# Performance work log

Measured on AMD Instinct MI355X. Metric: run time of the kernel, lower is better.

The kernel has to match this reference:

```python
import jax, jax.numpy as jnp
import numpy as np

N, E, G = 30000, 240000, 1500
EMB, NODE_DIM, EDGE_DIM, TASKS = 300, 9, 3, 12
L_ENC, L_RAT = 5, 2
GAMMA, T_CON = 0.4, 0.2


def _w(key, shape, fan_in):
    return jax.random.normal(key, shape, jnp.float32) / np.float32(np.sqrt(fan_in))


def setup_inputs() -> dict:
    key = jax.random.key(0)
    ks = jax.random.split(key, 32)
    inp = {}
    inp['x'] = jax.random.normal(ks[0], (N, NODE_DIM), jnp.float32)
    inp['edge_attr'] = jax.random.normal(ks[1], (E, EDGE_DIM), jnp.float32)
    inp['edge_index'] = jax.random.randint(ks[2], (2, E), 0, N, jnp.int32)
    b = jnp.sort(jax.random.randint(ks[3], (N,), 0, G, jnp.int32))
    inp['batch'] = b.at[0].set(0).at[-1].set(G - 1)
    u = jax.random.uniform(ks[4], (N, 2), jnp.float32, 1e-6, 1.0 - 1e-6)
    inp['gumbel'] = -jnp.log(-jnp.log(u))  # standard Gumbel noise (tau=1)
    inp['perm'] = jax.random.permutation(ks[5], G).astype(jnp.int32)
    inp['W_enc'] = _w(ks[6], (NODE_DIM, EMB), NODE_DIM)
    inp['b_enc'] = jnp.zeros((EMB,), jnp.float32)
    inp['We_g'] = _w(ks[7], (L_ENC, EDGE_DIM, EMB), EDGE_DIM)
    inp['be_g'] = jnp.zeros((L_ENC, EMB), jnp.float32)
    inp['W1_g'] = _w(ks[8], (L_ENC, EMB, 2 * EMB), EMB)
    inp['b1_g'] = jnp.zeros((L_ENC, 2 * EMB), jnp.float32)
    inp['W2_g'] = _w(ks[9], (L_ENC, 2 * EMB, EMB), 2 * EMB)
    inp['b2_g'] = jnp.zeros((L_ENC, EMB), jnp.float32)
    inp['We_r'] = _w(ks[10], (L_RAT, EDGE_DIM, EMB), EDGE_DIM)
    inp['be_r'] = jnp.zeros((L_RAT, EMB), jnp.float32)
    inp['W1_r'] = _w(ks[11], (L_RAT, EMB, 2 * EMB), EMB)
    inp['b1_r'] = jnp.zeros((L_RAT, 2 * EMB), jnp.float32)
    inp['W2_r'] = _w(ks[12], (L_RAT, 2 * EMB, EMB), 2 * EMB)
    inp['b2_r'] = jnp.zeros((L_RAT, EMB), jnp.float32)
    inp['Wg1'] = _w(ks[13], (EMB, 2 * EMB), EMB)
    inp['bg1'] = jnp.zeros((2 * EMB,), jnp.float32)
    inp['Wg2'] = _w(ks[14], (2 * EMB, 2), 2 * EMB)
    inp['bg2'] = jnp.zeros((2,), jnp.float32)
    inp['Wp1'] = _w(ks[15], (EMB, 2 * EMB), EMB)
    inp['bp1'] = jnp.zeros((2 * EMB,), jnp.float32)
    inp['Wp2'] = _w(ks[16], (2 * EMB, TASKS), 2 * EMB)
    inp['bp2'] = jnp.zeros((TASKS,), jnp.float32)
    return inp


def _gin_stack(x, src, dst, edge_attr, We, be, W1, b1, W2, b2):
    # GIN-style message passing with edge features, residual, JK='last'.
    L = We.shape[0]
    for l in range(L):
        e = edge_attr @ We[l] + be[l]                               # [E, EMB]
        msg = jax.nn.relu(x[src] + e)                                # gather [E, EMB]
        agg = jax.ops.segment_sum(msg, dst, num_segments=x.shape[0])  # scatter [N, EMB]
        h = jax.nn.relu((agg + x) @ W1[l] + b1[l]) @ W2[l] + b2[l]
        if l < L - 1:
            h = jax.nn.relu(h)
        x = x + h  # residual
    return x


def _mlp2(h, Wa, ba, Wb, bb):
    # Linear -> (BN=identity in eval) -> ReLU -> (Dropout=identity) -> Linear
    return jax.nn.relu(h @ Wa + ba) @ Wb + bb


def _forward(x, edge_attr, gumbel, W_enc, b_enc, We_g, be_g, W1_g, b1_g, W2_g, b2_g,
             We_r, be_r, W1_r, b1_r, W2_r, b2_r, Wg1, bg1, Wg2, bg2, Wp1, bp1, Wp2, bp2,
             edge_index, batch, perm):
    src, dst = edge_index[0], edge_index[1]
    cnt = jnp.clip(jax.ops.segment_sum(jnp.ones((x.shape[0],), jnp.float32), batch, num_segments=G), 1.0)[:, None]

    def gmean(v):
        return jax.ops.segment_sum(v, batch, num_segments=G) / cnt

    x_feat = x @ W_enc + b_enc                                      # node encoder
    h_node = _gin_stack(x_feat, src, dst, edge_attr, We_g, be_g, W1_g, b1_g, W2_g, b2_g)
    x_rat = _gin_stack(x_feat, src, dst, edge_attr, We_r, be_r, W1_r, b1_r, W2_r, b2_r)

    gate_logits = _mlp2(x_rat, Wg1, bg1, Wg2, bg2)                  # [N, 2]
    gate = jax.nn.softmax(gate_logits + gumbel, axis=-1)[:, 1:2]     # gumbel-softmax (soft), keep last col

    h_r = gmean(gate * h_node)
    h_env = gmean((1.0 - gate) * h_node)
    r_num = jax.ops.segment_sum(gate, batch, num_segments=G) + 1e-8
    env_num = jax.ops.segment_sum(1.0 - gate, batch, num_segments=G) + 1e-8

    pred_rem = _mlp2(h_r, Wp1, bp1, Wp2, bp2)
    loss_reg = jnp.abs(r_num / (r_num + env_num) - GAMMA).mean()

    h_out = gmean(h_node)
    na = jnp.linalg.norm(h_r, axis=1)
    nb = jnp.linalg.norm(h_out, axis=1)
    nc = jnp.linalg.norm(h_env, axis=1)
    sim = jnp.exp((h_r @ h_out.T) / (na[:, None] * nb[None, :] + 1e-8) / T_CON)
    sim_cp = jnp.exp((h_r @ h_env.T) / (na[:, None] * nc[None, :] + 1e-8) / T_CON)
    pos = jnp.diagonal(sim)
    loss_con = -jnp.log(pos / (sim_cp.sum(axis=1) + pos)).mean()

    pred_rep = _mlp2(h_r + h_env[perm], Wp1, bp1, Wp2, bp2)
    return pred_rep, pred_rem, loss_reg, loss_con


def reference(x, edge_attr, gumbel, W_enc, b_enc, We_g, be_g, W1_g, b1_g, W2_g, b2_g,
              We_r, be_r, W1_r, b1_r, W2_r, b2_r, Wg1, bg1, Wg2, bg2, Wp1, bp1, Wp2, bp2,
              edge_index, batch, perm):
    return _forward(x, edge_attr, gumbel, W_enc, b_enc, We_g, be_g, W1_g, b1_g, W2_g, b2_g,
                    We_r, be_r, W1_r, b1_r, W2_r, b2_r, Wg1, bg1, Wg2, bg2, Wp1, bp1, Wp2, bp2,
                    edge_index, batch, perm)
```

## Files before the change

### kernel.cpp

```cpp
#include <hip/hip_runtime.h>
#include <hip/hip_bf16.h>

typedef __hip_bfloat16 bf16;
typedef __attribute__((ext_vector_type(8))) short bf16x8;
typedef __attribute__((ext_vector_type(4))) float f32x4;

#define NN 30000
#define NE 240000
#define NG 1500
#define EMB 300
#define HID 600
#define NTASK 12
#define SEM 320
#define SHID 608
#define CG 75
#define NBLK_SCAN 118

__device__ __forceinline__ float tof(bf16 v){ return __bfloat162float(v); }
__device__ __forceinline__ bf16  tob(float v){ return __float2bfloat16(v); }
__device__ __forceinline__ float b2f(unsigned short u){ return __uint_as_float(((unsigned)u)<<16); }

__global__ __launch_bounds__(256) void k_hist(const int* __restrict__ dst, int* __restrict__ deg){
    int e = blockIdx.x*256 + threadIdx.x;
    if (e < NE) atomicAdd(&deg[dst[e]], 1);
}

__global__ __launch_bounds__(256) void k_scanA(const int* __restrict__ deg, int* __restrict__ bsum){
    __shared__ int red[256];
    int b = blockIdx.x, t = threadIdx.x;
    int i = b*256 + t;
    red[t] = (i < NN) ? deg[i] : 0;
    __syncthreads();
    for (int off=128; off>0; off>>=1){ if (t<off) red[t]+=red[t+off]; __syncthreads(); }
    if (t==0) bsum[b] = red[0];
}

__global__ __launch_bounds__(128) void k_scanB(const int* __restrict__ bsum, int* __restrict__ boff){
    __shared__ int s[128];
    int t = threadIdx.x;
    int v = (t < NBLK_SCAN) ? bsum[t] : 0;
    s[t] = v;
    __syncthreads();
    for (int off=1; off<128; off<<=1){
        int add = (t>=off) ? s[t-off] : 0;
        __syncthreads();
        s[t] += add;
        __syncthreads();
    }
    if (t < NBLK_SCAN) boff[t] = s[t] - v;
}

__global__ __launch_bounds__(256) void k_scanC(const int* __restrict__ deg, const int* __restrict__ boff,
                                               int* __restrict__ indptr, int* __restrict__ cursor){
    __shared__ int s[256];
    int b = blockIdx.x, t = threadIdx.x;
    int i = b*256 + t;
    int v = (i < NN) ? deg[i] : 0;
    s[t] = v;
    __syncthreads();
    for (int off=1; off<256; off<<=1){
        int add = (t>=off) ? s[t-off] : 0;
        __syncthreads();
        s[t] += add;
        __syncthreads();
    }
    int excl = s[t] - v + boff[b];
    if (i < NN){ indptr[i] = excl; cursor[i] = excl; }
    if (i == 0) indptr[NN] = NE;
}

__global__ __launch_bounds__(256) void k_scatter(const int* __restrict__ dst, int* __restrict__ cursor,
                                                 int* __restrict__ eid){
    int e = blockIdx.x*256 + threadIdx.x;
    if (e < NE){ int p = atomicAdd(&cursor[dst[e]], 1); eid[p] = e; }
}

__global__ __launch_bounds__(256) void k_eprep(const int* __restrict__ eid, const int* __restrict__ src,
                                               const float* __restrict__ eattr, float4* __restrict__ epack){
    int k = blockIdx.x*256 + threadIdx.x;
    if (k >= NE) return;
    int e = eid[k];
    float4 p;
    p.x = __int_as_float(src[e]);
    p.y = eattr[e*3]; p.z = eattr[e*3+1]; p.w = eattr[e*3+2];
    epack[k] = p;
}

__global__ __launch_bounds__(256) void k_wprep_all(
        const float* __restrict__ W1_g, const float* __restrict__ W2_g,
        const float* __restrict__ W1_r, const float* __restrict__ W2_r,
        const float* __restrict__ Wg1,  const float* __restrict__ Wp1,
        bf16* __restrict__ wt1g, bf16* __restrict__ wt2g,
        bf16* __restrict__ wt1r, bf16* __restrict__ wt2r,
        bf16* __restrict__ wtg1, bf16* __restrict__ wtp1,
        int* __restrict__ deg, const int* __restrict__ batch, int* __restrict__ gstart,
        const float* __restrict__ x, const float* __restrict__ W_enc,
        const float* __restrict__ b_enc, bf16* __restrict__ xfeat,
        float* __restrict__ glogit){
    __shared__ float t[32][33];
    int z = blockIdx.z;
    if (z >= 18){
        int idx = ((z-18)*361 + blockIdx.y*19 + blockIdx.x)*256 + threadIdx.x;
        if (idx >= NN*EMB) return;
        int n = idx / EMB, c = idx - n*EMB;
        float acc = b_enc[c];
        #pragma unroll
        for (int k=0;k<9;k++) acc += x[n*9+k] * W_enc[k*EMB+c];
        xfeat[(size_t)n*SEM + c] = tob(acc);
        return;
    }
    if (z == 16){
        int i = (blockIdx.y*19 + blockIdx.x)*256 + threadIdx.x;
        if (i < NN){ deg[i] = 0; glogit[2*i] = 0.f; glogit[2*i+1] = 0.f; }
        return;
    }
    if (z == 17){
        int g = (blockIdx.y*19 + blockIdx.x)*256 + threadIdx.x;
        if (g > NG) return;
        if (g == NG){ gstart[NG] = NN; return; }
        int lo=0, hi=NN;
        while (lo<hi){ int mid=(lo+hi)>>1; if (batch[mid] < g) lo=mid+1; else hi=mid; }
        gstart[g] = lo;
        return;
    }
    const float* Ws; bf16* Wd; int K, Kp, N;
    if (z < 5)      { Ws = W1_g + (size_t)z*EMB*HID;      Wd = wt1g + (size_t)z*HID*SEM;      K=EMB; Kp=SEM;  N=HID; }
    else if (z < 10){ int l=z-5;  Ws = W2_g + (size_t)l*HID*EMB; Wd = wt2g + (size_t)l*EMB*SHID; K=HID; Kp=SHID; N=EMB; }
    else if (z < 12){ int l=z-10; Ws = W1_r + (size_t)l*EMB*HID; Wd = wt1r + (size_t)l*HID*SEM;  K=EMB; Kp=SEM;  N=HID; }
    else if (z < 14){ int l=z-12; Ws = W2_r + (size_t)l*HID*EMB; Wd = wt2r + (size_t)l*EMB*SHID; K=HID; Kp=SHID; N=EMB; }
    else if (z ==14){ Ws = Wg1; Wd = wtg1; K=EMB; Kp=SEM; N=HID; }
    else            { Ws = Wp1; Wd = wtp1; K=EMB; Kp=SEM; N=HID; }
    int n0 = blockIdx.x*32, k0 = blockIdx.y*32;
    if (n0 >= N || k0 >= Kp) return;
    int tx = threadIdx.x & 31, ty = threadIdx.x >> 5;
    #pragma unroll
    for (int i=0;i<4;i++){
        int k = k0 + ty + i*8, n = n0 + tx;
        t[ty+i*8][tx] = (k<K && n<N) ? Ws[(size_t)k*N+n] : 0.f;
    }
    __syncthreads();
    #pragma unroll
    for (int i=0;i<4;i++){
        int n = n0 + ty + i*8, k = k0 + tx;
        if (n<N && k<Kp) Wd[(size_t)n*Kp+k] = tob(t[tx][ty+i*8]);
    }
}

__device__ __forceinline__ void agg4_body(const bf16* __restrict__ cur, const float* __restrict__ We,
                      const float* __restrict__ be, const float4* __restrict__ epack,
                      const int* __restrict__ indptr, bf16* __restrict__ apx, int idx){
    int n = idx / CG, cg = idx - n*CG;
    int c0 = cg*4;
    float w0[4], w1[4], w2[4], bbv[4], acc[4];
    #pragma unroll
    for (int j=0;j<4;j++){
        w0[j] = We[c0+j]; w1[j] = We[EMB+c0+j]; w2[j] = We[2*EMB+c0+j]; bbv[j] = be[c0+j];
    }
    ushort4 hs = *(const ushort4*)&cur[(size_t)n*SEM + c0];
    acc[0]=b2f(hs.x); acc[1]=b2f(hs.y); acc[2]=b2f(hs.z); acc[3]=b2f(hs.w);
    int k  = indptr[n], k1 = indptr[n+1];

    auto accum4 = [&](float4 e0, float4 e1, float4 e2, float4 e3,
                      ushort4 ha, ushort4 hb, ushort4 hc, ushort4 hd){
        float fa[4] = {b2f(ha.x), b2f(ha.y), b2f(ha.z), b2f(ha.w)};
        float fb[4] = {b2f(hb.x), b2f(hb.y), b2f(hb.z), b2f(hb.w)};
        float fc[4] = {b2f(hc.x), b2f(hc.y), b2f(hc.z), b2f(hc.w)};
        float fd[4] = {b2f(hd.x), b2f(hd.y), b2f(hd.z), b2f(hd.w)};
        #pragma unroll
        for (int j=0;j<4;j++){
            float va = fa[j] + e0.y*w0[j] + e0.z*w1[j] + e0.w*w2[j] + bbv[j];
            float vb = fb[j] + e1.y*w0[j] + e1.z*w1[j] + e1.w*w2[j] + bbv[j];
            float vc = fc[j] + e2.y*w0[j] + e2.z*w1[j] + e2.w*w2[j] + bbv[j];
            float vd = fd[j] + e3.y*w0[j] + e3.z*w1[j] + e3.w*w2[j] + bbv[j];
            acc[j] += fmaxf(va, 0.f) + fmaxf(vb, 0.f) + fmaxf(vc, 0.f) + fmaxf(vd, 0.f);
        }
    };

    if (k + 4 <= k1){
        float4 e0 = epack[k], e1 = epack[k+1], e2 = epack[k+2], e3 = epack[k+3];
        ushort4 h0 = *(const ushort4*)&cur[(size_t)__float_as_int(e0.x)*SEM + c0];
        ushort4 h1 = *(const ushort4*)&cur[(size_t)__float_as_int(e1.x)*SEM + c0];
        ushort4 h2 = *(const ushort4*)&cur[(size_t)__float_as_int(e2.x)*SEM + c0];
        ushort4 h3 = *(const ushort4*)&cur[(size_t)__float_as_int(e3.x)*SEM + c0];
        while (k + 8 <= k1){
            float4 f0 = epack[k+4], f1 = epack[k+5], f2 = epack[k+6], f3 = epack[k+7];
            ushort4 g0 = *(const ushort4*)&cur[(size_t)__float_as_int(f0.x)*SEM + c0];
            ushort4 g1 = *(const ushort4*)&cur[(size_t)__float_as_int(f1.x)*SEM + c0];
            ushort4 g2 = *(const ushort4*)&cur[(size_t)__float_as_int(f2.x)*SEM + c0];
            ushort4 g3 = *(const ushort4*)&cur[(size_t)__float_as_int(f3.x)*SEM + c0];
            accum4(e0,e1,e2,e3, h0,h1,h2,h3);
            e0=f0; e1=f1; e2=f2; e3=f3;
            h0=g0; h1=g1; h2=g2; h3=g3;
            k += 4;
        }
        accum4(e0,e1,e2,e3, h0,h1,h2,h3);
        k += 4;
    }
    for (; k < k1; k++){
        float4 e0 = epack[k];
        int s0 = __float_as_int(e0.x);
        ushort4 ha = *(const ushort4*)&cur[(size_t)s0*SEM + c0];
        float fa[4] = {b2f(ha.x), b2f(ha.y), b2f(ha.z), b2f(ha.w)};
        #pragma unroll
        for (int j=0;j<4;j++){
            float va = fa[j] + e0.y*w0[j] + e0.z*w1[j] + e0.w*w2[j] + bbv[j];
            acc[j] += fmaxf(va, 0.f);
        }
    }
    ushort4 o;
    o.x = __bfloat16_as_ushort(tob(acc[0]));
    o.y = __bfloat16_as_ushort(tob(acc[1]));
    o.z = __bfloat16_as_ushort(tob(acc[2]));
    o.w = __bfloat16_as_ushort(tob(acc[3]));
    *(ushort4*)&apx[(size_t)n*SEM + c0] = o;
}

__global__ __launch_bounds__(256) void k_agg4(const bf16* __restrict__ cur, const float* __restrict__ We,
                      const float* __restrict__ be, const float4* __restrict__ epack,
                      const int* __restrict__ indptr, bf16* __restrict__ apx){
    int idx = blockIdx.x*256 + threadIdx.x;
    if (idx >= NN*CG) return;
    agg4_body(cur, We, be, epack, indptr, apx, idx);
}

__global__ __launch_bounds__(256) void k_agg4z(const bf16* __restrict__ cur0, const bf16* __restrict__ cur1,
                      const float* __restrict__ We0, const float* __restrict__ We1,
                      const float* __restrict__ be0, const float* __restrict__ be1,
                      const float4* __restrict__ epack, const int* __restrict__ indptr,
                      bf16* __restrict__ apx0, bf16* __restrict__ apx1){
    int idx = blockIdx.x*256 + threadIdx.x;
    if (idx >= NN*CG) return;
    if (blockIdx.z == 0) agg4_body(cur0, We0, be0, epack, indptr, apx0, idx);
    else                 agg4_body(cur1, We1, be1, epack, indptr, apx1, idx);
}

__global__ __launch_bounds__(256) void k_agg4d(const bf16* __restrict__ cur,
                      const float* __restrict__ WeA, const float* __restrict__ beA,
                      const float* __restrict__ WeB, const float* __restrict__ beB,
// ... 26 lines not shown
        for (int j=0;j<4;j++){
            accA[j] += fmaxf(fa[j] + e0.y*a0[j] + e0.z*a1[j] + e0.w*a2[j] + ab[j], 0.f)
                     + fmaxf(fb[j] + e1.y*a0[j] + e1.z*a1[j] + e1.w*a2[j] + ab[j], 0.f);
            accB[j] += fmaxf(fa[j] + e0.y*b0[j] + e0.z*b1[j] + e0.w*b2[j] + bb[j], 0.f)
                     + fmaxf(fb[j] + e1.y*b0[j] + e1.z*b1[j] + e1.w*b2[j] + bb[j], 0.f);
        }
    }
    if (k < k1){
        float4 e0 = epack[k];
        int s0 = __float_as_int(e0.x);
        ushort4 ha = *(const ushort4*)&cur[(size_t)s0*SEM + c0];
        float fa[4] = {b2f(ha.x), b2f(ha.y), b2f(ha.z), b2f(ha.w)};
        #pragma unroll
        for (int j=0;j<4;j++){
            accA[j] += fmaxf(fa[j] + e0.y*a0[j] + e0.z*a1[j] + e0.w*a2[j] + ab[j], 0.f);
            accB[j] += fmaxf(fa[j] + e0.y*b0[j] + e0.z*b1[j] + e0.w*b2[j] + bb[j], 0.f);
        }
    }
    ushort4 oA, oB;
    oA.x=__bfloat16_as_ushort(tob(accA[0])); oA.y=__bfloat16_as_ushort(tob(accA[1]));
    oA.z=__bfloat16_as_ushort(tob(accA[2])); oA.w=__bfloat16_as_ushort(tob(accA[3]));
    oB.x=__bfloat16_as_ushort(tob(accB[0])); oB.y=__bfloat16_as_ushort(tob(accB[1]));
    oB.z=__bfloat16_as_ushort(tob(accB[2])); oB.w=__bfloat16_as_ushort(tob(accB[3]));
    *(ushort4*)&apxA[(size_t)n*SEM + c0] = oA;
    *(ushort4*)&apxB[(size_t)n*SEM + c0] = oB;
}

__device__ __forceinline__ void gemm_body(const bf16* __restrict__ A, const bf16* __restrict__ Bt,
        const float* __restrict__ bias, const bf16* __restrict__ R, bf16* __restrict__ C,
        int M, int N, int Kp, int ldc, int relu_out, short* lds, int m0, int n0){
    short* Ct = lds;
    const int CS = 136;
    int tid = threadIdx.x;
    int wave = tid >> 6, lane = tid & 63;
    int wm = wave >> 1, wn = wave & 1;

    int srow = tid >> 1;
    int sq   = (tid & 1) * 2;
    int grA = min(m0 + srow, M-1);
    int grB = min(n0 + srow, N-1);
    const bf16* pA = A  + (size_t)grA*Kp + sq*8;
    const bf16* pB = Bt + (size_t)grB*Kp + sq*8;
    int aoff0 = ((srow>>4)*64 +  sq   *16 + (srow&15))*8;
    int aoff1 = ((srow>>4)*64 + (sq+1)*16 + (srow&15))*8;

    f32x4 acc[4][4];
    #pragma unroll
    for (int i=0;i<4;i++){
        #pragma unroll
        for (int j=0;j<4;j++) acc[i][j] = (f32x4){0.f,0.f,0.f,0.f};
    }

    int KC = Kp >> 5;
    uint4 ra0 = *(const uint4*)(pA);
    uint4 ra1 = *(const uint4*)(pA + 8);
    uint4 rb0 = *(const uint4*)(pB);
    uint4 rb1 = *(const uint4*)(pB + 8);
    *(uint4*)(lds + aoff0)        = ra0;
    *(uint4*)(lds + aoff1)        = ra1;
    *(uint4*)(lds + 4096 + aoff0) = rb0;
    *(uint4*)(lds + 4096 + aoff1) = rb1;
    __syncthreads();
    if (KC > 1){
        ra0 = *(const uint4*)(pA + 32); ra1 = *(const uint4*)(pA + 40);
        rb0 = *(const uint4*)(pB + 32); rb1 = *(const uint4*)(pB + 40);
    }

    for (int kc=0; kc<KC; ++kc){
        short* cbuf = lds + (kc & 1)*8192;
        short* nbuf = lds + ((kc+1) & 1)*8192;
        if (kc+1 < KC){
            *(uint4*)(nbuf + aoff0)        = ra0;
            *(uint4*)(nbuf + aoff1)        = ra1;
            *(uint4*)(nbuf + 4096 + aoff0) = rb0;
            *(uint4*)(nbuf + 4096 + aoff1) = rb1;
            if (kc+2 < KC){
                const bf16* qA = pA + (kc+2)*32;
                const bf16* qB = pB + (kc+2)*32;
                ra0 = *(const uint4*)(qA); ra1 = *(const uint4*)(qA+8);
                rb0 = *(const uint4*)(qB); rb1 = *(const uint4*)(qB+8);
            }
        }
        bf16x8 af[4], bfr[4];
        #pragma unroll
        for (int i=0;i<4;i++) af[i]  = *(const bf16x8*)(cbuf + ((wm*4+i)*64 + lane)*8);
        #pragma unroll
        for (int j=0;j<4;j++) bfr[j] = *(const bf16x8*)(cbuf + 4096 + ((wn*4+j)*64 + lane)*8);
        #pragma unroll
        for (int i=0;i<4;i++){
            #pragma unroll
            for (int j=0;j<4;j++)
                acc[i][j] = __builtin_amdgcn_mfma_f32_16x16x32_bf16(af[i], bfr[j], acc[i][j], 0, 0, 0);
        }
        __syncthreads();
    }

    int lq = lane >> 4, lr = lane & 15;
    #pragma unroll
    for (int i=0;i<4;i++){
        int rl = (wm*4+i)*16 + lq*4;
        #pragma unroll
        for (int j=0;j<4;j++){
            int cl = (wn*4+j)*16 + lr;
            float bv = bias[min(n0+cl, N-1)];
            #pragma unroll
            for (int r=0;r<4;r++){
                float v = acc[i][j][r] + bv;
                if (relu_out) v = fmaxf(v, 0.f);
                Ct[(rl+r)*CS + cl] = (short)__bfloat16_as_ushort(tob(v));
            }
        }
    }
    __syncthreads();
    #pragma unroll
    for (int p=0;p<8;p++){
        int rl = p*16 + (tid>>4);
        int cl = (tid&15)*8;
        int row = m0 + rl, col = n0 + cl;
        if (row < M && col < N){
            union { short s8[8]; uint4 v; } u;
            u.v = *(uint4*)&Ct[rl*CS + cl];
            if (R){
                const bf16* rp = &R[(size_t)row*ldc + col];
                #pragma unroll
                for (int e=0;e<8;e++){
                    float v = b2f((unsigned short)u.s8[e]) + tof(rp[e]);
                    u.s8[e] = (short)__bfloat16_as_ushort(tob(v));
                }
            }
            *(uint4*)&C[(size_t)row*ldc + col] = u.v;
        }
    }
}

__global__ __launch_bounds__(256) void k_gemm2(const bf16* __restrict__ A, const bf16* __restrict__ Bt,
        const float* __restrict__ bias, const bf16* __restrict__ R, bf16* __restrict__ C,
        int M, int N, int Kp, int ldc, int relu_out){
    __shared__ __align__(16) char ldsbuf[34816];
    gemm_body(A, Bt, bias, R, C, M, N, Kp, ldc, relu_out, (short*)ldsbuf,
              blockIdx.y*128, blockIdx.x*128);
}

__global__ __launch_bounds__(256) void k_gemm2z(
        const bf16* __restrict__ A0, const bf16* __restrict__ A1,
        const bf16* __restrict__ Bt0, const bf16* __restrict__ Bt1,
        const float* __restrict__ bias0, const float* __restrict__ bias1,
        const bf16* __restrict__ R0, const bf16* __restrict__ R1,
        bf16* __restrict__ C0, bf16* __restrict__ C1,
        int M, int N, int Kp, int ldc, int relu0, int relu1){
    __shared__ __align__(16) char ldsbuf[34816];
    int m0 = blockIdx.y*128, n0 = blockIdx.x*128;
    if (blockIdx.z == 0) gemm_body(A0, Bt0, bias0, R0, C0, M, N, Kp, ldc, relu0, (short*)ldsbuf, m0, n0);
    else                 gemm_body(A1, Bt1, bias1, R1, C1, M, N, Kp, ldc, relu1, (short*)ldsbuf, m0, n0);
}

__device__ __forceinline__ void gemm64_body(const bf16* __restrict__ A, const bf16* __restrict__ Bt,
        const float* __restrict__ bias, const bf16* __restrict__ R, bf16* __restrict__ C,
        int M, int N, int Kp, int ldc, int relu_out, short* lds, int m0, int n0){
    short* Ct = lds;
    const int CS = 72;
    int tid = threadIdx.x;
    int wave = tid >> 6, lane = tid & 63;
    int wm = wave >> 1, wn = wave & 1;

    int srow = tid >> 1;
    int sq   = (tid & 1) * 2;
    int grA = min(m0 + srow, M-1);
    const bf16* pA = A + (size_t)grA*Kp + sq*8;
    int aoff0 = ((srow>>4)*64 +  sq   *16 + (srow&15))*8;
    int aoff1 = ((srow>>4)*64 + (sq+1)*16 + (srow&15))*8;

    int brow = tid >> 2;
    int bq   = tid & 3;
    int grB = min(n0 + brow, N-1);
    const bf16* pB = Bt + (size_t)grB*Kp + bq*8;
    int boff = ((brow>>4)*64 + bq*16 + (brow&15))*8;

    f32x4 acc[4][2];
    #pragma unroll
    for (int i=0;i<4;i++){
        #pragma unroll
        for (int j=0;j<2;j++) acc[i][j] = (f32x4){0.f,0.f,0.f,0.f};
    }

    int KC = Kp >> 5;
    uint4 ra0 = *(const uint4*)(pA);
    uint4 ra1 = *(const uint4*)(pA + 8);
    uint4 rb0 = *(const uint4*)(pB);
    *(uint4*)(lds + aoff0)       = ra0;
    *(uint4*)(lds + aoff1)       = ra1;
    *(uint4*)(lds + 4096 + boff) = rb0;
    __syncthreads();
    if (KC > 1){
        ra0 = *(const uint4*)(pA + 32); ra1 = *(const uint4*)(pA + 40);
        rb0 = *(const uint4*)(pB + 32);
    }

    for (int kc=0; kc<KC; ++kc){
        short* cbuf = lds + (kc & 1)*6144;
        short* nbuf = lds + ((kc+1) & 1)*6144;
        if (kc+1 < KC){
            *(uint4*)(nbuf + aoff0)       = ra0;
            *(uint4*)(nbuf + aoff1)       = ra1;
            *(uint4*)(nbuf + 4096 + boff) = rb0;
            if (kc+2 < KC){
                const bf16* qA = pA + (kc+2)*32;
                ra0 = *(const uint4*)(qA); ra1 = *(const uint4*)(qA+8);
                rb0 = *(const uint4*)(pB + (kc+2)*32);
            }
        }
        bf16x8 af[4], bfr[2];
        #pragma unroll
        for (int i=0;i<4;i++) af[i]  = *(const bf16x8*)(cbuf + ((wm*4+i)*64 + lane)*8);
        #pragma unroll
        for (int j=0;j<2;j++) bfr[j] = *(const bf16x8*)(cbuf + 4096 + ((wn*2+j)*64 + lane)*8);
        #pragma unroll
        for (int i=0;i<4;i++){
            #pragma unroll
            for (int j=0;j<2;j++)
                acc[i][j] = __builtin_amdgcn_mfma_f32_16x16x32_bf16(af[i], bfr[j], acc[i][j], 0, 0, 0);
        }
        __syncthreads();
    }

    int lq = lane >> 4, lr = lane & 15;
    #pragma unroll
    for (int i=0;i<4;i++){
        int rl = (wm*4+i)*16 + lq*4;
        #pragma unroll
        for (int j=0;j<2;j++){
            int cl = (wn*2+j)*16 + lr;
            float bv = bias[min(n0+cl, N-1)];
            #pragma unroll
            for (int r=0;r<4;r++){
                float v = acc[i][j][r] + bv;
                if (relu_out) v = fmaxf(v, 0.f);
                Ct[(rl+r)*CS + cl] = (short)__bfloat16_as_ushort(tob(v));
            }
        }
    }
    __syncthreads();
    #pragma unroll
    for (int p=0;p<4;p++){
        int rl = p*32 + (tid>>3);
        int cl = (tid&7)*8;
        int row = m0 + rl, col = n0 + cl;
        if (row < M && col < N){
            union { short s8[8]; uint4 v; } u;
            u.v = *(uint4*)&Ct[rl*CS + cl];
            if (R){
                const bf16* rp = &R[(size_t)row*ldc + col];
                #pragma unroll
                for (int e=0;e<8;e++){
                    float v = b2f((unsigned short)u.s8[e]) + tof(rp[e]);
                    u.s8[e] = (short)__bfloat16_as_ushort(tob(v));
                }
            }
            *(uint4*)&C[(size_t)row*ldc + col] = u.v;
        }
    }
}

__global__ __launch_bounds__(256) void k_gemm64(const bf16* __restrict__ A, const bf16* __restrict__ Bt,
        const float* __restrict__ bias, const bf16* __restrict__ R, bf16* __restrict__ C,
        int M, int N, int Kp, int ldc, int relu_out){
    __shared__ __align__(16) char ldsbuf[24576];
    gemm64_body(A, Bt, bias, R, C, M, N, Kp, ldc, relu_out, (short*)ldsbuf,
                blockIdx.y*128, blockIdx.x*64);
}

__global__ __launch_bounds__(256) void k_gemm64z(
        const bf16* __restrict__ A0, const bf16* __restrict__ A1,
        const bf16* __restrict__ Bt0, const bf16* __restrict__ Bt1,
        const float* __restrict__ bias0, const float* __restrict__ bias1,
        const bf16* __restrict__ R0, const bf16* __restrict__ R1,
        bf16* __restrict__ C0, bf16* __restrict__ C1,
        int M, int N, int Kp, int ldc, int relu0, int relu1){
    __shared__ __align__(16) char ldsbuf[24576];
    int m0 = blockIdx.y*128, n0 = blockIdx.x*64;
    if (blockIdx.z == 0) gemm64_body(A0, Bt0, bias0, R0, C0, M, N, Kp, ldc, relu0, (short*)ldsbuf, m0, n0);
    else                 gemm64_body(A1, Bt1, bias1, R1, C1, M, N, Kp, ldc, relu1, (short*)ldsbuf, m0, n0);
}

__device__ __forceinline__ void gate_gemm_body(const bf16* __restrict__ A, const bf16* __restrict__ Bt,
        const float* __restrict__ bias, const float* __restrict__ Wg2, float* __restrict__ glogit,
        int M, int N, int Kp, short* lds, int m0, int n0){
    int tid = threadIdx.x;
    int wave = tid >> 6, lane = tid & 63;
    int wm = wave >> 1, wn = wave & 1;

    int srow = tid >> 1;
    int sq   = (tid & 1) * 2;
    int grA = min(m0 + srow, M-1);
    int grB = min(n0 + srow, N-1);
    const bf16* pA = A  + (size_t)grA*Kp + sq*8;
    const bf16* pB = Bt + (size_t)grB*Kp + sq*8;
    int aoff0 = ((srow>>4)*64 +  sq   *16 + (srow&15))*8;
    int aoff1 = ((srow>>4)*64 + (sq+1)*16 + (srow&15))*8;

    f32x4 acc[4][4];
    #pragma unroll
    for (int i=0;i<4;i++){
        #pragma unroll
        for (int j=0;j<4;j++) acc[i][j] = (f32x4){0.f,0.f,0.f,0.f};
    }

    int KC = Kp >> 5;
    uint4 ra0 = *(const uint4*)(pA);
    uint4 ra1 = *(const uint4*)(pA + 8);
    uint4 rb0 = *(const uint4*)(pB);
    uint4 rb1 = *(const uint4*)(pB + 8);
    *(uint4*)(lds + aoff0)        = ra0;
    *(uint4*)(lds + aoff1)        = ra1;
    *(uint4*)(lds + 4096 + aoff0) = rb0;
    *(uint4*)(lds + 4096 + aoff1) = rb1;
    __syncthreads();
    if (KC > 1){
        ra0 = *(const uint4*)(pA + 32); ra1 = *(const uint4*)(pA + 40);
        rb0 = *(const uint4*)(pB + 32); rb1 = *(const uint4*)(pB + 40);
    }

    for (int kc=0; kc<KC; ++kc){
        short* cbuf = lds + (kc & 1)*8192;
        short* nbuf = lds + ((kc+1) & 1)*8192;
        if (kc+1 < KC){
            *(uint4*)(nbuf + aoff0)        = ra0;
            *(uint4*)(nbuf + aoff1)        = ra1;
            *(uint4*)(nbuf + 4096 + aoff0) = rb0;
            *(uint4*)(nbuf + 4096 + aoff1) = rb1;
            if (kc+2 < KC){
                const bf16* qA = pA + (kc+2)*32;
                const bf16* qB = pB + (kc+2)*32;
                ra0 = *(const uint4*)(qA); ra1 = *(const uint4*)(qA+8);
                rb0 = *(const uint4*)(qB); rb1 = *(const uint4*)(qB+8);
            }
        }
        bf16x8 af[4], bfr[4];
        #pragma unroll
        for (int i=0;i<4;i++) af[i]  = *(const bf16x8*)(cbuf + ((wm*4+i)*64 + lane)*8);
        #pragma unroll
        for (int j=0;j<4;j++) bfr[j] = *(const bf16x8*)(cbuf + 4096 + ((wn*4+j)*64 + lane)*8);
        #pragma unroll
        for (int i=0;i<4;i++){
            #pragma unroll
            for (int j=0;j<4;j++)
                acc[i][j] = __builtin_amdgcn_mfma_f32_16x16x32_bf16(af[i], bfr[j], acc[i][j], 0, 0, 0);
        }
        __syncthreads();
    }

    int lq = lane >> 4, lr = lane & 15;
    #pragma unroll
    for (int i=0;i<4;i++){
        #pragma unroll
        for (int r=0;r<4;r++){
            int row = m0 + (wm*4+i)*16 + lq*4 + r;
            float p0 = 0.f, p1 = 0.f;
            #pragma unroll
            for (int j=0;j<4;j++){
                int cl = (wn*4+j)*16 + lr;
                int col = n0 + cl;
                float v = fmaxf(acc[i][j][r] + bias[min(col, N-1)], 0.f);
                if (col < N){ p0 += v * Wg2[col*2]; p1 += v * Wg2[col*2+1]; }
            }
            #pragma unroll
            for (int m=1; m<16; m<<=1){ p0 += __shfl_xor(p0, m); p1 += __shfl_xor(p1, m); }
            if (lr == 0 && row < M){
                atomicAdd(&glogit[row*2],   p0);
                atomicAdd(&glogit[row*2+1], p1);
            }
        }
    }
}

__global__ __launch_bounds__(256) void k_gatepair(
        const bf16* __restrict__ Ag, const bf16* __restrict__ Btg, const float* __restrict__ bg,
        const float* __restrict__ Wg2, float* __restrict__ glogit,
        const bf16* __restrict__ A1, const bf16* __restrict__ Bt1, const float* __restrict__ b1,
        bf16* __restrict__ C1){
    __shared__ __align__(16) char ldsbuf[34816];
    int bid = blockIdx.x;
    if (bid < 1175){
        gate_gemm_body(Ag, Btg, bg, Wg2, glogit, NN, HID, SEM, (short*)ldsbuf,
                       (bid/5)*128, (bid%5)*128);
    } else {
        int gb = bid - 1175;
        gemm_body(A1, Bt1, b1, nullptr, C1, NN, HID, SEM, SHID, 1, (short*)ldsbuf,
                  (gb/5)*128, (gb%5)*128);
    }
}

__global__ __launch_bounds__(256) void k_gatefin(const float* __restrict__ glogit,
        const float* __restrict__ bg2, const float* __restrict__ gumbel, float* __restrict__ gate){
    int i = blockIdx.x*256 + threadIdx.x;
    if (i >= NN) return;
    float l0 = glogit[2*i]   + bg2[0] + gumbel[2*i];
    float l1 = glogit[2*i+1] + bg2[1] + gumbel[2*i+1];
    float m = fmaxf(l0, l1);
    float e0 = expf(l0-m), e1 = expf(l1-m);
    gate[i] = e1/(e0+e1);
}

__device__ __forceinline__ void stage_tile(const short* __restrict__ P, int RB, int K, int r0, int k0,
                                           short (*lds)[64][8], int tid){
    #pragma unroll
    for (int s=0;s<2;s++){
        int seg = tid*2+s;
        int row = seg>>2, q = seg&3;
        int gr = r0 + row;
        int gk = k0 + q*8;
        union { short s8[8]; uint4 v; } u;
        if (gr < RB && gk + 8 <= K){
            const uint2* p = (const uint2*)(P + (size_t)gr*K + gk);
            uint2 lo = p[0], hi = p[1];
            u.v.x = lo.x; u.v.y = lo.y; u.v.z = hi.x; u.v.w = hi.y;
        } else {
            #pragma unroll
            for (int j=0;j<8;j++){
                int kk = gk + j;
                u.s8[j] = (gr < RB && kk < K) ? P[(size_t)gr*K + kk] : (short)0;
            }
        }
        *(uint4*)&lds[row>>4][q*16 + (row&15)][0] = u.v;
    }
}

__device__ __forceinline__ void sim_body(const bf16* __restrict__ A, const bf16* __restrict__ Bt,
                      const float* __restrict__ na, const float* __restrict__ nc, float* __restrict__ S,
                      char* ldsraw){
    short (*Asl)[64][8] = (short(*)[64][8])ldsraw;
    short (*Bsl)[64][8] = (short(*)[64][8])(ldsraw + 8192);
    int tid = threadIdx.x;
    int wave = tid >> 6, lane = tid & 63;
    int wm = wave >> 1, wn = wave & 1;
// ... 95 lines not shown
        if (c == 319) Ssum[g] = 0.f;
    }
    float srr=r*r, soo=o*o, see=e*e, sro=r*o;
    #pragma unroll
    for (int off=32; off>0; off>>=1){
        srr += __shfl_down(srr,off); soo += __shfl_down(soo,off);
        see += __shfl_down(see,off); sro += __shfl_down(sro,off);
    }
    __shared__ float ws[4][5];
    int wv = c >> 6, ln = c & 63;
    if (ln == 0){ ws[0][wv]=srr; ws[1][wv]=soo; ws[2][wv]=see; ws[3][wv]=sro; }
    __syncthreads();
    if (c == 0){
        float a=0.f,b=0.f,c2=0.f,d=0.f;
        #pragma unroll
        for (int i=0;i<5;i++){ a+=ws[0][i]; b+=ws[1][i]; c2+=ws[2][i]; d+=ws[3][i]; }
        float sa = sqrtf(a), sb = sqrtf(b), sc = sqrtf(c2);
        na[g] = sa; nc[g] = sc;
        pos[g] = expf(d/(sa*sb + 1e-8f) * 5.0f);
    }
}

__global__ __launch_bounds__(256) void k_pbuild2(const float* __restrict__ hr, const float* __restrict__ henv,
                      const int* __restrict__ perm, bf16* __restrict__ P){
    int idx = blockIdx.x*256 + threadIdx.x;
    if (idx >= NG*SEM) return;
    int g = idx / SEM, c = idx - g*SEM;
    P[(size_t)(NG+g)*SEM + c] = (c < EMB)
        ? tob(hr[g*EMB+c] + henv[(size_t)perm[g]*EMB + c])
        : tob(0.f);
}

__global__ __launch_bounds__(256) void k_pred(const bf16* __restrict__ hidP, const float* __restrict__ Wp2,
                      const float* __restrict__ bp2, float* __restrict__ out){
    int r = blockIdx.x*4 + (threadIdx.x >> 6);
    int lane = threadIdx.x & 63;
    if (r >= 2*NG) return;
    float acc[NTASK];
    #pragma unroll
    for (int t=0;t<NTASK;t++) acc[t] = 0.f;
    for (int i=lane;i<HID;i+=64){
        float h = tof(hidP[(size_t)r*SHID+i]);
        const float4* wp = (const float4*)&Wp2[i*NTASK];
        float4 wa = wp[0], wb = wp[1], wc = wp[2];
        acc[0]+=h*wa.x; acc[1]+=h*wa.y; acc[2]+=h*wa.z; acc[3]+=h*wa.w;
        acc[4]+=h*wb.x; acc[5]+=h*wb.y; acc[6]+=h*wb.z; acc[7]+=h*wb.w;
        acc[8]+=h*wc.x; acc[9]+=h*wc.y; acc[10]+=h*wc.z; acc[11]+=h*wc.w;
    }
    #pragma unroll
    for (int t=0;t<NTASK;t++){
        for (int off=32; off>0; off>>=1) acc[t] += __shfl_down(acc[t], off);
    }
    if (lane==0){
        float* dst = (r < NG) ? &out[NG*NTASK + r*NTASK] : &out[(r-NG)*NTASK];
        #pragma unroll
        for (int t=0;t<NTASK;t++) dst[t] = acc[t] + bp2[t];
    }
}

__global__ __launch_bounds__(256) void k_loss(const float* __restrict__ cntf, const float* __restrict__ rnum,
                      const float* __restrict__ pos, const float* __restrict__ S, float* __restrict__ out){
    __shared__ float ra[256], rb[256];
    int t = threadIdx.x;
    float a=0.f, b=0.f;
    for (int g=t; g<NG; g+=256){
        float r = rnum[g] + 1e-8f;
        float e = (cntf[g] - rnum[g]) + 1e-8f;
        a += fabsf(r/(r+e) - 0.4f);
        float p = pos[g];
        b += -logf(p/(S[g]+p));
    }
    ra[t]=a; rb[t]=b; __syncthreads();
    for (int off=128; off>0; off>>=1){ if (t<off){ ra[t]+=ra[t+off]; rb[t]+=rb[t+off]; } __syncthreads(); }
    if (t==0){
        out[2*NG*NTASK]   = ra[0]/NG;
        out[2*NG*NTASK+1] = rb[0]/NG;
    }
}

extern "C" void kernel_launch(void* const* d_in, const int* in_sizes, int n_in,
                              void* d_out, int out_size, void* d_ws, size_t ws_size,
                              hipStream_t stream) {
    const float* x      = (const float*)d_in[0];
    const float* eattr  = (const float*)d_in[1];
    const int*   eidx   = (const int*)d_in[2];
    const int*   batch  = (const int*)d_in[3];
    const float* gumbel = (const float*)d_in[4];
    const int*   perm   = (const int*)d_in[5];
    const float* W_enc  = (const float*)d_in[6];
    const float* b_enc  = (const float*)d_in[7];
    const float* We_g   = (const float*)d_in[8];
    const float* be_g   = (const float*)d_in[9];
    const float* W1_g   = (const float*)d_in[10];
    const float* b1_g   = (const float*)d_in[11];
    const float* W2_g   = (const float*)d_in[12];
    const float* b2_g   = (const float*)d_in[13];
    const float* We_r   = (const float*)d_in[14];
    const float* be_r   = (const float*)d_in[15];
    const float* W1_r   = (const float*)d_in[16];
    const float* b1_r   = (const float*)d_in[17];
    const float* W2_r   = (const float*)d_in[18];
    const float* b2_r   = (const float*)d_in[19];
    const float* Wg1    = (const float*)d_in[20];
    const float* bg1    = (const float*)d_in[21];
    const float* Wg2    = (const float*)d_in[22];
    const float* bg2    = (const float*)d_in[23];
    const float* Wp1    = (const float*)d_in[24];
    const float* bp1    = (const float*)d_in[25];
    const float* Wp2    = (const float*)d_in[26];
    const float* bp2    = (const float*)d_in[27];
    float* out = (float*)d_out;

    const int* srcArr = eidx;
    const int* dstArr = eidx + NE;

    char* w = (char*)d_ws;
    size_t off = 0;
    auto alloc = [&](size_t bytes)->char*{ char* p = w + off; off += (bytes + 255) & ~(size_t)255; return p; };
    bf16* xfeat = (bf16*)alloc((size_t)NN*SEM*2);
    bf16* cur_r = (bf16*)alloc((size_t)NN*SEM*2);
    bf16* cur_g = (bf16*)alloc((size_t)NN*SEM*2);
    bf16* apx   = (bf16*)alloc((size_t)NN*SEM*2);
    bf16* apx2  = (bf16*)alloc((size_t)NN*SEM*2);
    char* midc  = alloc((size_t)NN*SHID*2);
    bf16* mid_r = (bf16*)midc;
    bf16* Pbuf   = (bf16*)(midc + 12*1024*1024);
    bf16* hidP   = (bf16*)(midc + 20*1024*1024);
    bf16* mid_g = (bf16*)alloc((size_t)NN*SHID*2);
    bf16* wt1g  = (bf16*)alloc((size_t)5*HID*SEM*2);
    bf16* wt2g  = (bf16*)alloc((size_t)5*EMB*SHID*2);
    bf16* wt1r  = (bf16*)alloc((size_t)2*HID*SEM*2);
    bf16* wt2r  = (bf16*)alloc((size_t)2*EMB*SHID*2);
    bf16* wtg1  = (bf16*)alloc((size_t)HID*SEM*2);
    bf16* wtp1  = (bf16*)alloc((size_t)HID*SEM*2);
    float4* epack = (float4*)alloc((size_t)NE*16);
    float* gate  = (float*)alloc((size_t)NN*4);
    float* glogit= (float*)alloc((size_t)NN*2*4);
    float* sumh  = (float*)alloc((size_t)NG*EMB*4);
    float* sumgh = (float*)alloc((size_t)NG*EMB*4);
    float* hr    = (float*)alloc((size_t)NG*EMB*4);
    float* henv  = (float*)alloc((size_t)NG*EMB*4);
    float* hout  = (float*)alloc((size_t)NG*EMB*4);
    bf16* hrb    = (bf16*)alloc((size_t)NG*SEM*2);
    bf16* henvb  = (bf16*)alloc((size_t)NG*SEM*2);
    float* rnum  = (float*)alloc(NG*4);
    float* cntf  = (float*)alloc(NG*4);
    float* na    = (float*)alloc(NG*4);
    float* ncv   = (float*)alloc(NG*4);
    float* pos   = (float*)alloc(NG*4);
    float* Ssum  = (float*)alloc(NG*4);
    int* deg     = (int*)alloc((size_t)NN*4);
    int* indptr  = (int*)alloc((size_t)(NN+1)*4);
    int* cursor  = (int*)alloc((size_t)NN*4);
    int* eid     = (int*)alloc((size_t)NE*4);
    int* gstart  = (int*)alloc((size_t)(NG+1)*4);
    int* bsum    = (int*)alloc((size_t)NBLK_SCAN*4);
    int* boff    = (int*)alloc((size_t)NBLK_SCAN*4);

    const int NB_NE  = (NE+255)/256;
    const int NB_AG  = (NN*CG+255)/256;
    const int NB_GP  = (NG*SEM+255)/256;

    dim3 gwp(19, 19, 18 + 98);
    k_wprep_all<<<gwp, 256, 0, stream>>>(W1_g, W2_g, W1_r, W2_r, Wg1, Wp1,
                                         wt1g, wt2g, wt1r, wt2r, wtg1, wtp1,
                                         deg, batch, gstart, x, W_enc, b_enc, xfeat, glogit);

    k_hist   <<<NB_NE, 256, 0, stream>>>(dstArr, deg);
    k_scanA  <<<NBLK_SCAN, 256, 0, stream>>>(deg, bsum);
    k_scanB  <<<1, 128, 0, stream>>>(bsum, boff);
    k_scanC  <<<NBLK_SCAN, 256, 0, stream>>>(deg, boff, indptr, cursor);
    k_scatter<<<NB_NE, 256, 0, stream>>>(dstArr, cursor, eid);
    k_eprep  <<<NB_NE, 256, 0, stream>>>(eid, srcArr, eattr, epack);

    dim3 gm1z((HID+127)/128, (NN+127)/128, 2);
    dim3 gm64z((EMB+63)/64, (NN+127)/128, 2);
    dim3 gm1((HID+127)/128, (NN+127)/128);
    dim3 gm64((EMB+63)/64, (NN+127)/128);
    dim3 gagz(NB_AG, 1, 2);

    k_agg4d<<<NB_AG, 256, 0, stream>>>(xfeat, We_r, be_r, We_g, be_g, epack, indptr, apx, apx2);
    k_gemm2z<<<gm1z, 256, 0, stream>>>(apx, apx2, wt1r, wt1g, b1_r, b1_g,
                                       nullptr, nullptr, mid_r, mid_g, NN, HID, SEM, SHID, 1, 1);
    k_gemm64z<<<gm64z, 256, 0, stream>>>(mid_r, mid_g, wt2r, wt2g, b2_r, b2_g,
                                         xfeat, xfeat, cur_r, cur_g, NN, EMB, SHID, SEM, 1, 1);

    k_agg4z<<<gagz, 256, 0, stream>>>(cur_r, cur_g, We_r + 3*EMB, We_g + 3*EMB, be_r + EMB, be_g + EMB,
                                      epack, indptr, apx, apx2);
    k_gemm2z<<<gm1z, 256, 0, stream>>>(apx, apx2, wt1r + (size_t)HID*SEM, wt1g + (size_t)HID*SEM,
                                       b1_r + HID, b1_g + HID, nullptr, nullptr, mid_r, mid_g,
                                       NN, HID, SEM, SHID, 1, 1);
    k_gemm64z<<<gm64z, 256, 0, stream>>>(mid_r, mid_g, wt2r + (size_t)EMB*SHID, wt2g + (size_t)EMB*SHID,
                                         b2_r + EMB, b2_g + EMB, cur_r, cur_g, cur_r, cur_g,
                                         NN, EMB, SHID, SEM, 0, 1);

    k_agg4 <<<NB_AG, 256, 0, stream>>>(cur_g, We_g + 2*3*EMB, be_g + 2*EMB, epack, indptr, apx2);
    k_gatepair<<<2350, 256, 0, stream>>>(cur_r, wtg1, bg1, Wg2, glogit,
                                         apx2, wt1g + (size_t)2*HID*SEM, b1_g + 2*HID, mid_g);
    k_gatefin<<<(NN+255)/256, 256, 0, stream>>>(glogit, bg2, gumbel, gate);
    k_gemm64<<<gm64, 256, 0, stream>>>(mid_g, wt2g + (size_t)2*EMB*SHID, b2_g + 2*EMB, cur_g, cur_g,
                                       NN, EMB, SHID, SEM, 1);

    for (int l=3; l<5; l++){
        k_agg4 <<<NB_AG, 256, 0, stream>>>(cur_g, We_g + l*3*EMB, be_g + l*EMB, epack, indptr, apx2);
        k_gemm2<<<gm1, 256, 0, stream>>>(apx2, wt1g + (size_t)l*HID*SEM, b1_g + l*HID, nullptr, mid_g,
                                         NN, HID, SEM, SHID, 1);
        k_gemm64<<<gm64, 256, 0, stream>>>(mid_g, wt2g + (size_t)l*EMB*SHID, b2_g + l*EMB, cur_g, cur_g,
                                           NN, EMB, SHID, SEM, (l<4)?1:0);
    }

    k_pool    <<<NG, 320, 0, stream>>>(cur_g, gate, gstart, sumh, sumgh, rnum, cntf);
    k_meannorm<<<NG, 320, 0, stream>>>(sumh, sumgh, cntf, hr, henv, hout, hrb, henvb, Pbuf,
                                       na, ncv, pos, Ssum);
    k_pbuild2 <<<NB_GP, 256, 0, stream>>>(hr, henv, perm, Pbuf);
    dim3 gsh(12, 24, 2);
    k_simhead<<<gsh, 256, 0, stream>>>(hrb, henvb, na, ncv, Ssum, Pbuf, wtp1, bp1, hidP);
    k_pred  <<<(2*NG+3)/4, 256, 0, stream>>>(hidP, Wp2, bp2, out);
    k_loss  <<<1, 256, 0, stream>>>(cntf, rnum, pos, Ssum, out);
}
```

Baseline: 1.005 ms.

## Fuse edge scatter with packing and use 128-wide GEMM tiles for second MLP layer

Merges the CSR scatter and edge-pack kernels, so each edge writes its packed src/attr record straight to its sorted slot, dropping the eid buffer and one launch. Replaces the 128x64-tile GEMM used for the 600->300 projection with the existing 128x128-tile GEMM. The grid width goes from 5 to 3 column blocks, which cuts A re-reads but pads the last tile to 384 columns and launches fewer blocks. The scatter fusion makes packed-record writes random rather than coalesced.

New measurement: 942.7 us. 1.07x faster.

```diff
diff --git a/kernel.cpp b/kernel.cpp
--- a/kernel.cpp
+++ b/kernel.cpp
@@ -69,21 +69,15 @@
     if (i == 0) indptr[NN] = NE;
 }
 
-__global__ __launch_bounds__(256) void k_scatter(const int* __restrict__ dst, int* __restrict__ cursor,
-                                                 int* __restrict__ eid){
+__global__ __launch_bounds__(256) void k_scatterprep(const int* __restrict__ dst, const int* __restrict__ src,
+                      const float* __restrict__ eattr, int* __restrict__ cursor, float4* __restrict__ epack){
     int e = blockIdx.x*256 + threadIdx.x;
-    if (e < NE){ int p = atomicAdd(&cursor[dst[e]], 1); eid[p] = e; }
-}
-
-__global__ __launch_bounds__(256) void k_eprep(const int* __restrict__ eid, const int* __restrict__ src,
-                                               const float* __restrict__ eattr, float4* __restrict__ epack){
-    int k = blockIdx.x*256 + threadIdx.x;
-    if (k >= NE) return;
-    int e = eid[k];
-    float4 p;
-    p.x = __int_as_float(src[e]);
-    p.y = eattr[e*3]; p.z = eattr[e*3+1]; p.w = eattr[e*3+2];
-    epack[k] = p;
+    if (e >= NE) return;
+    int p = atomicAdd(&cursor[dst[e]], 1);
+    float4 q;
+    q.x = __int_as_float(src[e]);
+    q.y = eattr[e*3]; q.z = eattr[e*3+1]; q.w = eattr[e*3+2];
+    epack[p] = q;
 }
 
 __global__ __launch_bounds__(256) void k_wprep_all(
@@ -416,134 +410,6 @@
     int m0 = blockIdx.y*128, n0 = blockIdx.x*128;
     if (blockIdx.z == 0) gemm_body(A0, Bt0, bias0, R0, C0, M, N, Kp, ldc, relu0, (short*)ldsbuf, m0, n0);
     else                 gemm_body(A1, Bt1, bias1, R1, C1, M, N, Kp, ldc, relu1, (short*)ldsbuf, m0, n0);
-}
-
-__device__ __forceinline__ void gemm64_body(const bf16* __restrict__ A, const bf16* __restrict__ Bt,
-        const float* __restrict__ bias, const bf16* __restrict__ R, bf16* __restrict__ C,
-        int M, int N, int Kp, int ldc, int relu_out, short* lds, int m0, int n0){
-    short* Ct = lds;
-    const int CS = 72;
-    int tid = threadIdx.x;
-    int wave = tid >> 6, lane = tid & 63;
-    int wm = wave >> 1, wn = wave & 1;
-
-    int srow = tid >> 1;
-    int sq   = (tid & 1) * 2;
-    int grA = min(m0 + srow, M-1);
-    const bf16* pA = A + (size_t)grA*Kp + sq*8;
-    int aoff0 = ((srow>>4)*64 +  sq   *16 + (srow&15))*8;
-    int aoff1 = ((srow>>4)*64 + (sq+1)*16 + (srow&15))*8;
-
-    int brow = tid >> 2;
-    int bq   = tid & 3;
-    int grB = min(n0 + brow, N-1);
-    const bf16* pB = Bt + (size_t)grB*Kp + bq*8;
-    int boff = ((brow>>4)*64 + bq*16 + (brow&15))*8;
-
-    f32x4 acc[4][2];
-    #pragma unroll
-    for (int i=0;i<4;i++){
-        #pragma unroll
-        for (int j=0;j<2;j++) acc[i][j] = (f32x4){0.f,0.f,0.f,0.f};
-    }
-
-    int KC = Kp >> 5;
-    uint4 ra0 = *(const uint4*)(pA);
-    uint4 ra1 = *(const uint4*)(pA + 8);
-    uint4 rb0 = *(const uint4*)(pB);
-    *(uint4*)(lds + aoff0)       = ra0;
-    *(uint4*)(lds + aoff1)       = ra1;
-    *(uint4*)(lds + 4096 + boff) = rb0;
-    __syncthreads();
-    if (KC > 1){
-        ra0 = *(const uint4*)(pA + 32); ra1 = *(const uint4*)(pA + 40);
-        rb0 = *(const uint4*)(pB + 32);
-    }
-
-    for (int kc=0; kc<KC; ++kc){
-        short* cbuf = lds + (kc & 1)*6144;
-        short* nbuf = lds + ((kc+1) & 1)*6144;
-        if (kc+1 < KC){
-            *(uint4*)(nbuf + aoff0)       = ra0;
-            *(uint4*)(nbuf + aoff1)       = ra1;
-            *(uint4*)(nbuf + 4096 + boff) = rb0;
-            if (kc+2 < KC){
-                const bf16* qA = pA + (kc+2)*32;
-                ra0 = *(const uint4*)(qA); ra1 = *(const uint4*)(qA+8);
-                rb0 = *(const uint4*)(pB + (kc+2)*32);
-            }
-        }
-        bf16x8 af[4], bfr[2];
-        #pragma unroll
-        for (int i=0;i<4;i++) af[i]  = *(const bf16x8*)(cbuf + ((wm*4+i)*64 + lane)*8);
-        #pragma unroll
-        for (int j=0;j<2;j++) bfr[j] = *(const bf16x8*)(cbuf + 4096 + ((wn*2+j)*64 + lane)*8);
-        #pragma unroll
-        for (int i=0;i<4;i++){
-            #pragma unroll
-            for (int j=0;j<2;j++)
-                acc[i][j] = __builtin_amdgcn_mfma_f32_16x16x32_bf16(af[i], bfr[j], acc[i][j], 0, 0, 0);
-        }
-        __syncthreads();
-    }
-
-    int lq = lane >> 4, lr = lane & 15;
-    #pragma unroll
-    for (int i=0;i<4;i++){
-        int rl = (wm*4+i)*16 + lq*4;
-        #pragma unroll
-        for (int j=0;j<2;j++){
-            int cl = (wn*2+j)*16 + lr;
-            float bv = bias[min(n0+cl, N-1)];
-            #pragma unroll
-            for (int r=0;r<4;r++){
-                float v = acc[i][j][r] + bv;
-                if (relu_out) v = fmaxf(v, 0.f);
-                Ct[(rl+r)*CS + cl] = (short)__bfloat16_as_ushort(tob(v));
-            }
-        }
-    }
-    __syncthreads();
-    #pragma unroll
-    for (int p=0;p<4;p++){
-        int rl = p*32 + (tid>>3);
-        int cl = (tid&7)*8;
-        int row = m0 + rl, col = n0 + cl;
-        if (row < M && col < N){
-            union { short s8[8]; uint4 v; } u;
-            u.v = *(uint4*)&Ct[rl*CS + cl];
-            if (R){
-                const bf16* rp = &R[(size_t)row*ldc + col];
-                #pragma unroll
-                for (int e=0;e<8;e++){
-                    float v = b2f((unsigned short)u.s8[e]) + tof(rp[e]);
-                    u.s8[e] = (short)__bfloat16_as_ushort(tob(v));
-                }
-            }
-            *(uint4*)&C[(size_t)row*ldc + col] = u.v;
-        }
-    }
-}
-
-__global__ __launch_bounds__(256) void k_gemm64(const bf16* __restrict__ A, const bf16* __restrict__ Bt,
-        const float* __restrict__ bias, const bf16* __restrict__ R, bf16* __restrict__ C,
-        int M, int N, int Kp, int ldc, int relu_out){
-    __shared__ __align__(16) char ldsbuf[24576];
-    gemm64_body(A, Bt, bias, R, C, M, N, Kp, ldc, relu_out, (short*)ldsbuf,
-                blockIdx.y*128, blockIdx.x*64);
-}
-
-__global__ __launch_bounds__(256) void k_gemm64z(
-        const bf16* __restrict__ A0, const bf16* __restrict__ A1,
-        const bf16* __restrict__ Bt0, const bf16* __restrict__ Bt1,
-        const float* __restrict__ bias0, const float* __restrict__ bias1,
-        const bf16* __restrict__ R0, const bf16* __restrict__ R1,
-        bf16* __restrict__ C0, bf16* __restrict__ C1,
-        int M, int N, int Kp, int ldc, int relu0, int relu1){
-    __shared__ __align__(16) char ldsbuf[24576];
-    int m0 = blockIdx.y*128, n0 = blockIdx.x*64;
-    if (blockIdx.z == 0) gemm64_body(A0, Bt0, bias0, R0, C0, M, N, Kp, ldc, relu0, (short*)ldsbuf, m0, n0);
-    else                 gemm64_body(A1, Bt1, bias1, R1, C1, M, N, Kp, ldc, relu1, (short*)ldsbuf, m0, n0);
 }
 
 __device__ __forceinline__ void gate_gemm_body(const bf16* __restrict__ A, const bf16* __restrict__ Bt,
@@ -945,7 +811,6 @@
     int* deg     = (int*)alloc((size_t)NN*4);
     int* indptr  = (int*)alloc((size_t)(NN+1)*4);
     int* cursor  = (int*)alloc((size_t)NN*4);
-    int* eid     = (int*)alloc((size_t)NE*4);
     int* gstart  = (int*)alloc((size_t)(NG+1)*4);
     int* bsum    = (int*)alloc((size_t)NBLK_SCAN*4);
     int* boff    = (int*)alloc((size_t)NBLK_SCAN*4);
@@ -959,47 +824,46 @@
                                          wt1g, wt2g, wt1r, wt2r, wtg1, wtp1,
                                          deg, batch, gstart, x, W_enc, b_enc, xfeat, glogit);
 
-    k_hist   <<<NB_NE, 256, 0, stream>>>(dstArr, deg);
-    k_scanA  <<<NBLK_SCAN, 256, 0, stream>>>(deg, bsum);
-    k_scanB  <<<1, 128, 0, stream>>>(bsum, boff);
-    k_scanC  <<<NBLK_SCAN, 256, 0, stream>>>(deg, boff, indptr, cursor);
-    k_scatter<<<NB_NE, 256, 0, stream>>>(dstArr, cursor, eid);
-    k_eprep  <<<NB_NE, 256, 0, stream>>>(eid, srcArr, eattr, epack);
+    k_hist       <<<NB_NE, 256, 0, stream>>>(dstArr, deg);
+    k_scanA      <<<NBLK_SCAN, 256, 0, stream>>>(deg, bsum);
+    k_scanB      <<<1, 128, 0, stream>>>(bsum, boff);
+    k_scanC      <<<NBLK_SCAN, 256, 0, stream>>>(deg, boff, indptr, cursor);
+    k_scatterprep<<<NB_NE, 256, 0, stream>>>(dstArr, srcArr, eattr, cursor, epack);
 
     dim3 gm1z((HID+127)/128, (NN+127)/128, 2);
-    dim3 gm64z((EMB+63)/64, (NN+127)/128, 2);
+    dim3 gm2z((EMB+127)/128, (NN+127)/128, 2);
     dim3 gm1((HID+127)/128, (NN+127)/128);
-    dim3 gm64((EMB+63)/64, (NN+127)/128);
+    dim3 gm2((EMB+127)/128, (NN+127)/128);
     dim3 gagz(NB_AG, 1, 2);
 
     k_agg4d<<<NB_AG, 256, 0, stream>>>(xfeat, We_r, be_r, We_g, be_g, epack, indptr, apx, apx2);
     k_gemm2z<<<gm1z, 256, 0, stream>>>(apx, apx2, wt1r, wt1g, b1_r, b1_g,
                                        nullptr, nullptr, mid_r, mid_g, NN, HID, SEM, SHID, 1, 1);
-    k_gemm64z<<<gm64z, 256, 0, stream>>>(mid_r, mid_g, wt2r, wt2g, b2_r, b2_g,
-                                         xfeat, xfeat, cur_r, cur_g, NN, EMB, SHID, SEM, 1, 1);
+    k_gemm2z<<<gm2z, 256, 0, stream>>>(mid_r, mid_g, wt2r, wt2g, b2_r, b2_g,
+                                       xfeat, xfeat, cur_r, cur_g, NN, EMB, SHID, SEM, 1, 1);
 
     k_agg4z<<<gagz, 256, 0, stream>>>(cur_r, cur_g, We_r + 3*EMB, We_g + 3*EMB, be_r + EMB, be_g + EMB,
                                       epack, indptr, apx, apx2);
     k_gemm2z<<<gm1z, 256, 0, stream>>>(apx, apx2, wt1r + (size_t)HID*SEM, wt1g + (size_t)HID*SEM,
                                        b1_r + HID, b1_g + HID, nullptr, nullptr, mid_r, mid_g,
                                        NN, HID, SEM, SHID, 1, 1);
-    k_gemm64z<<<gm64z, 256, 0, stream>>>(mid_r, mid_g, wt2r + (size_t)EMB*SHID, wt2g + (size_t)EMB*SHID,
-                                         b2_r + EMB, b2_g + EMB, cur_r, cur_g, cur_r, cur_g,
-                                         NN, EMB, SHID, SEM, 0, 1);
+    k_gemm2z<<<gm2z, 256, 0, stream>>>(mid_r, mid_g, wt2r + (size_t)EMB*SHID, wt2g + (size_t)EMB*SHID,
+                                       b2_r + EMB, b2_g + EMB, cur_r, cur_g, cur_r, cur_g,
+                                       NN, EMB, SHID, SEM, 0, 1);
 
     k_agg4 <<<NB_AG, 256, 0, stream>>>(cur_g, We_g + 2*3*EMB, be_g + 2*EMB, epack, indptr, apx2);
     k_gatepair<<<2350, 256, 0, stream>>>(cur_r, wtg1, bg1, Wg2, glogit,
                                          apx2, wt1g + (size_t)2*HID*SEM, b1_g + 2*HID, mid_g);
     k_gatefin<<<(NN+255)/256, 256, 0, stream>>>(glogit, bg2, gumbel, gate);
-    k_gemm64<<<gm64, 256, 0, stream>>>(mid_g, wt2g + (size_t)2*EMB*SHID, b2_g + 2*EMB, cur_g, cur_g,
-                                       NN, EMB, SHID, SEM, 1);
+    k_gemm2<<<gm2, 256, 0, stream>>>(mid_g, wt2g + (size_t)2*EMB*SHID, b2_g + 2*EMB, cur_g, cur_g,
+                                     NN, EMB, SHID, SEM, 1);
 
     for (int l=3; l<5; l++){
         k_agg4 <<<NB_AG, 256, 0, stream>>>(cur_g, We_g + l*3*EMB, be_g + l*EMB, epack, indptr, apx2);
         k_gemm2<<<gm1, 256, 0, stream>>>(apx2, wt1g + (size_t)l*HID*SEM, b1_g + l*HID, nullptr, mid_g,
                                          NN, HID, SEM, SHID, 1);
-        k_gemm64<<<gm64, 256, 0, stream>>>(mid_g, wt2g + (size_t)l*EMB*SHID, b2_g + l*EMB, cur_g, cur_g,
-                                           NN, EMB, SHID, SEM, (l<4)?1:0);
+        k_gemm2<<<gm2, 256, 0, stream>>>(mid_g, wt2g + (size_t)l*EMB*SHID, b2_g + l*EMB, cur_g, cur_g,
+                                         NN, EMB, SHID, SEM, (l<4)?1:0);
     }
 
     k_pool    <<<NG, 320, 0, stream>>>(cur_g, gate, gstart, sumh, sumgh, rnum, cntf);
```
